# Optimization experiments

Hardware: AMD Instinct MI355X
Metric: run time of the kernel (lower is better)

The kernel has to match this reference:

```python
import jax, jax.numpy as jnp
import numpy as np

_IDENTITY = jnp.array([1, 0, 0, 0], dtype=jnp.float32)

G, T, P, B = 512, 128, 256, 512  # num_graphs, max_terms, n_params, batch


def setup_inputs() -> dict:
    key = jax.random.key(0)
    k0, k1, k2, k3, k4 = jax.random.split(key, 5)
    psi_const = jax.random.randint(k0, (G, T), 0, 2).astype(jnp.int32)
    psi_params = jax.random.randint(k1, (G, T, P), 0, 2).astype(jnp.float32)
    phi_const = jax.random.randint(k2, (G, T), 0, 2).astype(jnp.int32)
    phi_params = jax.random.randint(k3, (G, T, P), 0, 2).astype(jnp.float32)
    param_vals = jax.random.randint(k4, (B, P), 0, 2).astype(jnp.float32)
    return {
        "psi_const": psi_const,
        "psi_params": psi_params,
        "phi_const": phi_const,
        "phi_params": phi_params,
        "param_vals": param_vals,
    }


def reference(psi_const, psi_params, phi_const, phi_params, param_vals):
    # GF(2) matmul: contract bitmasks with binary parameter values, mod 2.
    # psi_params: (G,T,P), param_vals: (B,P) -> (B,G,T)
    psi = jnp.mod(psi_const[None].astype(jnp.float32)
                  + jnp.einsum("gtp,bp->bgt", psi_params, param_vals), 2.0)
    phi = jnp.mod(phi_const[None].astype(jnp.float32)
                  + jnp.einsum("gtp,bp->bgt", phi_params, param_vals), 2.0)
    # Elementwise parity product and mod-2 sum over terms -> (B,G)
    exponent = jnp.mod(psi * phi, 2.0)
    sum_exponents = jnp.mod(jnp.sum(exponent, axis=-1), 2.0)
    # Parity-to-sign: (-1)^e = 1 - 2e, embedded as exact scalar (B,G,4)
    summands_exact = (1.0 - 2.0 * sum_exponents)[..., None] * _IDENTITY
    return summands_exact
```

## Files before the change

### kernel.cpp

```cpp
#include <hip/hip_runtime.h>

typedef unsigned long long u64;

#define G 512
#define T 128
#define P 256
#define B 512

#define PV_OFF    0
#define ROWS_OFF  16384
#define CODES_OFF (ROWS_OFF + (size_t)G * T * 8 * 8)
#define WS_NEEDED (CODES_OFF + (size_t)G * T * 4)


#define ROWS_TOTAL (G * T * 2)
#define TPW        8
#define ROW_BLOCKS (ROWS_TOTAL / (TPW * 4))
#define PV_BLOCKS  (B / (TPW * 4))
#define PACK_BLOCKS (ROW_BLOCKS + PV_BLOCKS)

__global__ __launch_bounds__(256) void pack_all_kernel(
    const int*   __restrict__ psi_const,
    const float* __restrict__ psi_params,
    const int*   __restrict__ phi_const,
    const float* __restrict__ phi_params,
    const float* __restrict__ pv,
    u64*         __restrict__ rows_ws,
    unsigned*    __restrict__ codes_ws,
    u64*         __restrict__ pv_ws)
{
    int gtid = blockIdx.x * 256 + threadIdx.x;
    if (gtid < G * T) {
        unsigned pc = ((unsigned)psi_const[gtid]) & 1u;
        unsigned qc = ((unsigned)phi_const[gtid]) & 1u;
        codes_ws[gtid] = pc | (qc << 1);
    }

    const int lane = threadIdx.x & 63;
    const int wvin = threadIdx.x >> 6;

    const float* srcb;
    u64*         dstb;
    size_t       dst_stride;
    if (blockIdx.x < ROW_BLOCKS) {
        int base = (blockIdx.x * 4 + wvin) * TPW;
        int mat  = base >> 16;
        int idx  = base & (G * T - 1);
        srcb = (mat ? phi_params : psi_params) + (size_t)idx * P;
        dstb = rows_ws + (size_t)idx * 8 + mat * 4;
        dst_stride = 8;
    } else {
        int brow = ((blockIdx.x - ROW_BLOCKS) * 4 + wvin) * TPW;
        srcb = pv + (size_t)brow * P;
        dstb = pv_ws + (size_t)brow * 4;
        dst_stride = 4;
    }

    const float4* src = (const float4*)srcb;
    float4 f[TPW];
    #pragma unroll
    for (int i = 0; i < TPW; ++i)
        f[i] = src[i * (P / 4) + lane];

    u64 w[TPW][4];
    #pragma unroll
    for (int i = 0; i < TPW; ++i) {
        w[i][0] = __ballot(f[i].x != 0.0f);
        w[i][1] = __ballot(f[i].y != 0.0f);
        w[i][2] = __ballot(f[i].z != 0.0f);
        w[i][3] = __ballot(f[i].w != 0.0f);
    }

    if (lane == 0) {
        #pragma unroll
        for (int i = 0; i < TPW; ++i) {
            ulonglong2* d = (ulonglong2*)(dstb + (size_t)i * dst_stride);
            d[0] = make_ulonglong2(w[i][0], w[i][1]);
            d[1] = make_ulonglong2(w[i][2], w[i][3]);
        }
    }
}

__global__ __launch_bounds__(512) void pi_trans_kernel(
    const u64*      __restrict__ rows,
    const unsigned* __restrict__ codes,
    const u64*      __restrict__ pv,
    float4*         __restrict__ out)
{
    const int g    = blockIdx.x;
    const int lane = threadIdx.x & 63;
    const int wv   = threadIdx.x >> 6;

    const u64* Rg = rows + (size_t)g * (T * 8);

    u64 ra[8], rb[8];
    {
        const ulonglong2* p0 = (const ulonglong2*)(Rg + (size_t)lane * 8);
        const ulonglong2* p1 = (const ulonglong2*)(Rg + (size_t)(lane + 64) * 8);
        #pragma unroll
        for (int q = 0; q < 4; ++q) { ulonglong2 x = p0[q]; ra[2*q] = x.x; ra[2*q+1] = x.y; }
        #pragma unroll
        for (int q = 0; q < 4; ++q) { ulonglong2 x = p1[q]; rb[2*q] = x.x; rb[2*q+1] = x.y; }
    }
    unsigned ca = codes[g * T + lane];
    unsigned cb = codes[g * T + lane + 64];
    unsigned pa = ca & 1u, qa = (ca >> 1) & 1u;
    unsigned pb = cb & 1u, qb = (cb >> 1) & 1u;

    #pragma unroll
    for (int grp = 0; grp < 2; ++grp) {
        int b0  = wv * 64 + grp * 32;
        int b0u = __builtin_amdgcn_readfirstlane(b0);
        const u64* vp = pv + (size_t)b0u * 4;

        unsigned acc = 0;
        #pragma unroll
        for (int i = 0; i < 32; ++i) {
            u64 v0 = vp[i * 4 + 0], v1 = vp[i * 4 + 1];
            u64 v2 = vp[i * 4 + 2], v3 = vp[i * 4 + 3];
            u64 m0 = (ra[0] & v0) ^ (ra[1] & v1) ^ (ra[2] & v2) ^ (ra[3] & v3);
            u64 m1 = (ra[4] & v0) ^ (ra[5] & v1) ^ (ra[6] & v2) ^ (ra[7] & v3);
            u64 m2 = (rb[0] & v0) ^ (rb[1] & v1) ^ (rb[2] & v2) ^ (rb[3] & v3);
            u64 m3 = (rb[4] & v0) ^ (rb[5] & v1) ^ (rb[6] & v2) ^ (rb[7] & v3);
            unsigned f0 = (unsigned)m0 ^ (unsigned)(m0 >> 32);
            unsigned f1 = (unsigned)m1 ^ (unsigned)(m1 >> 32);
            unsigned f2 = (unsigned)m2 ^ (unsigned)(m2 >> 32);
            unsigned f3 = (unsigned)m3 ^ (unsigned)(m3 >> 32);
            unsigned t01 = ((unsigned)__popc(f0) ^ pa) & ((unsigned)__popc(f1) ^ qa);
            unsigned t23 = ((unsigned)__popc(f2) ^ pb) & ((unsigned)__popc(f3) ^ qb);
            acc ^= ((t01 ^ t23) & 1u) << i;
        }

        unsigned red = acc;
        #pragma unroll
        for (int m = 1; m < 64; m <<= 1)
            red ^= __shfl_xor(red, m, 64);

        if (lane < 32) {
            int b = b0u + lane;
            float s = 1.0f - 2.0f * (float)((red >> lane) & 1u);
            out[(size_t)b * G + g] = make_float4(s, 0.0f, 0.0f, 0.0f);
        }
    }
}

struct __align__(16) U64x2 { u64 x, y; };

__global__ __launch_bounds__(256) void pack_pv_kernel(
    const float* __restrict__ pv, u64* __restrict__ out)
{
    int lane = threadIdx.x & 63;
    int wave = threadIdx.x >> 6;
    int row  = blockIdx.x * 4 + wave;
    const float4* src = (const float4*)(pv + (size_t)row * P);
    float4 f = src[lane];
    u64 w0 = __ballot(f.x != 0.0f);
    u64 w1 = __ballot(f.y != 0.0f);
    u64 w2 = __ballot(f.z != 0.0f);
    u64 w3 = __ballot(f.w != 0.0f);
    if (lane == 0) {
        out[row * 4 + 0] = w0;
        out[row * 4 + 1] = w1;
        out[row * 4 + 2] = w2;
        out[row * 4 + 3] = w3;
    }
}

__global__ __launch_bounds__(512) void pi_main_kernel(
    const int*   __restrict__ psi_const,
    const float* __restrict__ psi_params,
    const int*   __restrict__ phi_const,
    const float* __restrict__ phi_params,
    const u64*   __restrict__ pv,
    float4*      __restrict__ out)
{
    __shared__ __align__(16) u64 rows[T * 8];
    __shared__ unsigned code_sm[T];

    const int g    = blockIdx.x;
    const int tid  = threadIdx.x;
    const int lane = tid & 63;
    const int wave = tid >> 6;

    if (tid < T) {
        unsigned pc = ((unsigned)psi_const[g * T + tid]) & 1u;
        unsigned qc = ((unsigned)phi_const[g * T + tid]) & 1u;
        code_sm[tid] = pc | (qc << 1);
    }

    for (int i = 0; i < 32; ++i) {
        int r = wave * 32 + i;
        int t = r & (T - 1);
        const float* mat = (r < T) ? psi_params : phi_params;
        int off = (r < T) ? 0 : 4;
        const float4* src = (const float4*)(mat + ((size_t)g * T + t) * P);
        float4 f = src[lane];
        u64 w0 = __ballot(f.x != 0.0f);
        u64 w1 = __ballot(f.y != 0.0f);
        u64 w2 = __ballot(f.z != 0.0f);
        u64 w3 = __ballot(f.w != 0.0f);
        if (lane == 0) {
            U64x2* d = (U64x2*)&rows[t * 8 + off];
            U64x2 a; a.x = w0; a.y = w1;
            U64x2 c; c.x = w2; c.y = w3;
            d[0] = a;
            d[1] = c;
        }
    }
    __syncthreads();

    const int b = tid;
    const u64* v = pv + (size_t)b * 4;
    u64 v0 = v[0], v1 = v[1], v2 = v[2], v3 = v[3];

    unsigned e = 0;
    #pragma unroll 8
    for (int t = 0; t < T; ++t) {
        const U64x2* row = (const U64x2*)&rows[t * 8];
        U64x2 p0 = row[0], p1 = row[1], q0 = row[2], q1 = row[3];
        u64 ma = (p0.x & v0) ^ (p0.y & v1) ^ (p1.x & v2) ^ (p1.y & v3);
        u64 mb = (q0.x & v0) ^ (q0.y & v1) ^ (q1.x & v2) ^ (q1.y & v3);
        unsigned c = code_sm[t];
        e ^= (((unsigned)__popcll(ma) ^ c) & ((unsigned)__popcll(mb) ^ (c >> 1)));
    }
    e &= 1u;

    float s = 1.0f - 2.0f * (float)e;
    out[(size_t)b * G + g] = make_float4(s, 0.0f, 0.0f, 0.0f);
}

extern "C" void kernel_launch(void* const* d_in, const int* in_sizes, int n_in,
                              void* d_out, int out_size, void* d_ws, size_t ws_size,
                              hipStream_t stream) {
    const int*   psi_const  = (const int*)  d_in[0];
    const float* psi_params = (const float*)d_in[1];
    const int*   phi_const  = (const int*)  d_in[2];
    const float* phi_params = (const float*)d_in[3];
    const float* param_vals = (const float*)d_in[4];

    if (ws_size >= WS_NEEDED) {
        u64*      pv_ws    = (u64*)((char*)d_ws + PV_OFF);
        u64*      rows_ws  = (u64*)((char*)d_ws + ROWS_OFF);
        unsigned* codes_ws = (unsigned*)((char*)d_ws + CODES_OFF);

        pack_all_kernel<<<PACK_BLOCKS, 256, 0, stream>>>(
            psi_const, psi_params, phi_const, phi_params, param_vals,
            rows_ws, codes_ws, pv_ws);
        pi_trans_kernel<<<G, 512, 0, stream>>>(
            rows_ws, codes_ws, pv_ws, (float4*)d_out);
    } else {
        u64* pv_packed = (u64*)d_ws;
        pack_pv_kernel<<<B / 4, 256, 0, stream>>>(param_vals, pv_packed);
        pi_main_kernel<<<G, 512, 0, stream>>>(psi_const, psi_params,
                                              phi_const, phi_params,
                                              pv_packed, (float4*)d_out);
    }
}
```

Before: 188.3 us.

## Pack parameter bitmasks per-thread into separate psi/phi word buffers

Replaces the wave-ballot packing kernel with one where each thread reads 64 consecutive floats and builds a 64-bit mask with integer nonzero tests. Psi and phi masks go to separate workspace arrays, and the transpose kernel reads them from there. The aim is to cut ballot and cross-lane overhead and to remove the single-lane stores. The cost is that per-thread 256-byte strided reads may coalesce less well than the old wave-contiguous loads. The integer test also treats negative zero as nonzero.

After: 191.4 us. No clear change (+1.6%).

```diff
diff --git a/kernel.cpp b/kernel.cpp
--- a/kernel.cpp
+++ b/kernel.cpp
@@ -8,81 +8,83 @@
 #define B 512
 
 #define PV_OFF    0
-#define ROWS_OFF  16384
-#define CODES_OFF (ROWS_OFF + (size_t)G * T * 8 * 8)
+#define PSI_OFF   16384
+#define PHI_OFF   (PSI_OFF + (size_t)G * T * 4 * 8)
+#define CODES_OFF (PHI_OFF + (size_t)G * T * 4 * 8)
 #define WS_NEEDED (CODES_OFF + (size_t)G * T * 4)
 
 
-#define ROWS_TOTAL (G * T * 2)
-#define TPW        8
-#define ROW_BLOCKS (ROWS_TOTAL / (TPW * 4))
-#define PV_BLOCKS  (B / (TPW * 4))
-#define PACK_BLOCKS (ROW_BLOCKS + PV_BLOCKS)
-
-__global__ __launch_bounds__(256) void pack_all_kernel(
+#define PSI_W (G * T * P / 64)
+#define PHI_W PSI_W
+#define PV_W  (B * P / 64)
+#define TOTW  (PSI_W + PHI_W + PV_W)
+#define PACK2_BLOCKS (TOTW / 256)
+
+__device__ __forceinline__ unsigned nzbit(unsigned u) {
+    return (u | (0u - u)) >> 31;
+}
+
+__global__ __launch_bounds__(256) void pack_words_kernel(
     const int*   __restrict__ psi_const,
+    const int*   __restrict__ phi_const,
     const float* __restrict__ psi_params,
-    const int*   __restrict__ phi_const,
     const float* __restrict__ phi_params,
     const float* __restrict__ pv,
-    u64*         __restrict__ rows_ws,
-    unsigned*    __restrict__ codes_ws,
-    u64*         __restrict__ pv_ws)
-{
-    int gtid = blockIdx.x * 256 + threadIdx.x;
-    if (gtid < G * T) {
-        unsigned pc = ((unsigned)psi_const[gtid]) & 1u;
-        unsigned qc = ((unsigned)phi_const[gtid]) & 1u;
-        codes_ws[gtid] = pc | (qc << 1);
-    }
-
-    const int lane = threadIdx.x & 63;
-    const int wvin = threadIdx.x >> 6;
-
-    const float* srcb;
-    u64*         dstb;
-    size_t       dst_stride;
-    if (blockIdx.x < ROW_BLOCKS) {
-        int base = (blockIdx.x * 4 + wvin) * TPW;
-        int mat  = base >> 16;
-        int idx  = base & (G * T - 1);
-        srcb = (mat ? phi_params : psi_params) + (size_t)idx * P;
-        dstb = rows_ws + (size_t)idx * 8 + mat * 4;
-        dst_stride = 8;
+    u64*         __restrict__ psi_ws,
+    u64*         __restrict__ phi_ws,
+    u64*         __restrict__ pv_ws,
+    unsigned*    __restrict__ codes_ws)
+{
+    const int tid = blockIdx.x * 256 + threadIdx.x;
+
+    if (tid < G * T) {
+        unsigned pc = ((unsigned)psi_const[tid]) & 1u;
+        unsigned qc = ((unsigned)phi_const[tid]) & 1u;
+        codes_ws[tid] = pc | (qc << 1);
+    }
+
+    const float* s;
+    u64*         d;
+    if (tid < PSI_W) {
+        s = psi_params + (size_t)tid * 64;
+        d = psi_ws + tid;
+    } else if (tid < PSI_W + PHI_W) {
+        int w = tid - PSI_W;
+        s = phi_params + (size_t)w * 64;
+        d = phi_ws + w;
     } else {
-        int brow = ((blockIdx.x - ROW_BLOCKS) * 4 + wvin) * TPW;
-        srcb = pv + (size_t)brow * P;
-        dstb = pv_ws + (size_t)brow * 4;
-        dst_stride = 4;
-    }
-
-    const float4* src = (const float4*)srcb;
-    float4 f[TPW];
-    #pragma unroll
-    for (int i = 0; i < TPW; ++i)
-        f[i] = src[i * (P / 4) + lane];
-
-    u64 w[TPW][4];
-    #pragma unroll
-    for (int i = 0; i < TPW; ++i) {
-        w[i][0] = __ballot(f[i].x != 0.0f);
-        w[i][1] = __ballot(f[i].y != 0.0f);
-        w[i][2] = __ballot(f[i].z != 0.0f);
-        w[i][3] = __ballot(f[i].w != 0.0f);
-    }
-
-    if (lane == 0) {
-        #pragma unroll
-        for (int i = 0; i < TPW; ++i) {
-            ulonglong2* d = (ulonglong2*)(dstb + (size_t)i * dst_stride);
-            d[0] = make_ulonglong2(w[i][0], w[i][1]);
-            d[1] = make_ulonglong2(w[i][2], w[i][3]);
-        }
-    }
+        int w = tid - PSI_W - PHI_W;
+        s = pv + (size_t)w * 64;
+        d = pv_ws + w;
+    }
+
+    const uint4* sv = (const uint4*)s;
+    uint4 f[16];
+    #pragma unroll
+    for (int i = 0; i < 16; ++i) f[i] = sv[i];
+    __builtin_amdgcn_sched_barrier(0);
+
+    unsigned lo = 0, hi = 0;
+    #pragma unroll
+    for (int i = 0; i < 8; ++i) {
+        lo |= nzbit(f[i].x) << (4 * i + 0);
+        lo |= nzbit(f[i].y) << (4 * i + 1);
+        lo |= nzbit(f[i].z) << (4 * i + 2);
+        lo |= nzbit(f[i].w) << (4 * i + 3);
+    }
+    #pragma unroll
+    for (int i = 8; i < 16; ++i) {
+        hi |= nzbit(f[i].x) << (4 * (i - 8) + 0);
+        hi |= nzbit(f[i].y) << (4 * (i - 8) + 1);
+        hi |= nzbit(f[i].z) << (4 * (i - 8) + 2);
+        hi |= nzbit(f[i].w) << (4 * (i - 8) + 3);
+    }
+    *d = ((u64)hi << 32) | (u64)lo;
 }
 
 __global__ __launch_bounds__(512) void pi_trans_kernel(
-    const u64*      __restrict__ rows,
+    const u64*      __restrict__ psi_ws,
+    const u64*      __restrict__ phi_ws,
     const unsigned* __restrict__ codes,
     const u64*      __restrict__ pv,
     float4*         __restrict__ out)
@@ -91,16 +93,21 @@
     const int lane = threadIdx.x & 63;
     const int wv   = threadIdx.x >> 6;
 
-    const u64* Rg = rows + (size_t)g * (T * 8);
-
     u64 ra[8], rb[8];
     {
-        const ulonglong2* p0 = (const ulonglong2*)(Rg + (size_t)lane * 8);
-        const ulonglong2* p1 = (const ulonglong2*)(Rg + (size_t)(lane + 64) * 8);
-        #pragma unroll
-        for (int q = 0; q < 4; ++q) { ulonglong2 x = p0[q]; ra[2*q] = x.x; ra[2*q+1] = x.y; }
-        #pragma unroll
-        for (int q = 0; q < 4; ++q) { ulonglong2 x = p1[q]; rb[2*q] = x.x; rb[2*q+1] = x.y; }
+        const ulonglong2* pA0 = (const ulonglong2*)(psi_ws + ((size_t)g * T + lane) * 4);
+        const ulonglong2* pB0 = (const ulonglong2*)(phi_ws + ((size_t)g * T + lane) * 4);
+        const ulonglong2* pA1 = (const ulonglong2*)(psi_ws + ((size_t)g * T + lane + 64) * 4);
+        const ulonglong2* pB1 = (const ulonglong2*)(phi_ws + ((size_t)g * T + lane + 64) * 4);
+        ulonglong2 x;
+        x = pA0[0]; ra[0] = x.x; ra[1] = x.y;
+        x = pA0[1]; ra[2] = x.x; ra[3] = x.y;
+        x = pB0[0]; ra[4] = x.x; ra[5] = x.y;
+        x = pB0[1]; ra[6] = x.x; ra[7] = x.y;
+        x = pA1[0]; rb[0] = x.x; rb[1] = x.y;
+        x = pA1[1]; rb[2] = x.x; rb[3] = x.y;
+        x = pB1[0]; rb[4] = x.x; rb[5] = x.y;
+        x = pB1[1]; rb[6] = x.x; rb[7] = x.y;
     }
     unsigned ca = codes[g * T + lane];
     unsigned cb = codes[g * T + lane + 64];
@@ -240,14 +247,15 @@
 
     if (ws_size >= WS_NEEDED) {
         u64*      pv_ws    = (u64*)((char*)d_ws + PV_OFF);
-        u64*      rows_ws  = (u64*)((char*)d_ws + ROWS_OFF);
+        u64*      psi_ws   = (u64*)((char*)d_ws + PSI_OFF);
+        u64*      phi_ws   = (u64*)((char*)d_ws + PHI_OFF);
         unsigned* codes_ws = (unsigned*)((char*)d_ws + CODES_OFF);
 
-        pack_all_kernel<<<PACK_BLOCKS, 256, 0, stream>>>(
-            psi_const, psi_params, phi_const, phi_params, param_vals,
-            rows_ws, codes_ws, pv_ws);
+        pack_words_kernel<<<PACK2_BLOCKS, 256, 0, stream>>>(
+            psi_const, phi_const, psi_params, phi_params, param_vals,
+            psi_ws, phi_ws, pv_ws, codes_ws);
         pi_trans_kernel<<<G, 512, 0, stream>>>(
-            rows_ws, codes_ws, pv_ws, (float4*)d_out);
+            psi_ws, phi_ws, codes_ws, pv_ws, (float4*)d_out);
     } else {
         u64* pv_packed = (u64*)d_ws;
         pack_pv_kernel<<<B / 4, 256, 0, stream>>>(param_vals, pv_packed);
```
